# Kernel optimization log

Hardware: AMD Instinct MI355X
Metric: run time of the kernel (lower is better)

## Reference

```python
import jax, jax.numpy as jnp
import numpy as np

B, N, DEG = 64, 256, 16          # graphs, nodes per graph, avg degree
FIN, OUT, DEP, HID = 256, 256, 64, 256
E = B * N * DEG                   # 262144 edges (no self loops)
NN = B * N                        # 16384 total nodes


def setup_inputs() -> dict:
    key = jax.random.key(0)
    ks = jax.random.split(key, 12)
    s = 0.05
    x = jax.random.normal(ks[0], (NN, FIN), jnp.float32)
    # random edges within each graph block, guaranteed no self loops
    src = jax.random.randint(ks[1], (E,), 0, N)
    dst = (src + jax.random.randint(ks[2], (E,), 1, N)) % N
    gid = jnp.repeat(jnp.arange(B) * N, N * DEG)
    edge_index = jnp.stack([src + gid, dst + gid]).astype(jnp.int32)
    edge_attr = jax.random.normal(ks[3], (E, DEP), jnp.float32)
    WA = jax.random.normal(ks[4], (OUT, FIN), jnp.float32) * s
    WB = jax.random.normal(ks[5], (OUT, DEP), jnp.float32) * s
    gcn_bias = jnp.zeros((OUT,), jnp.float32)

    def gru_p(k, insz):
        k1, k2, k3, k4 = jax.random.split(k, 4)
        return (jax.random.normal(k1, (3 * HID, insz), jnp.float32) * s,
                jax.random.normal(k2, (3 * HID, HID), jnp.float32) * s,
                jax.random.normal(k3, (3 * HID,), jnp.float32) * s,
                jax.random.normal(k4, (3 * HID,), jnp.float32) * s)

    w_ih0, w_hh0, b_ih0, b_hh0 = gru_p(ks[6], OUT)
    w_ih1, w_hh1, b_ih1, b_hh1 = gru_p(ks[7], HID)
    w_ih2, w_hh2, b_ih2, b_hh2 = gru_p(ks[8], HID)
    lin_W = jax.random.normal(ks[9], (2, 5 * HID), jnp.float32) * s
    lin_b = jnp.zeros((2,), jnp.float32)
    return dict(x=x, edge_attr=edge_attr, edge_index=edge_index, WA=WA, WB=WB,
                gcn_bias=gcn_bias,
                w_ih0=w_ih0, w_hh0=w_hh0, b_ih0=b_ih0, b_hh0=b_hh0,
                w_ih1=w_ih1, w_hh1=w_hh1, b_ih1=b_ih1, b_hh1=b_hh1,
                w_ih2=w_ih2, w_hh2=w_hh2, b_ih2=b_ih2, b_hh2=b_hh2,
                lin_W=lin_W, lin_b=lin_b)


def _gru_layer(seq, w_ih, w_hh, b_ih, b_hh):
    # seq: [B, T, in] -> ([B, T, HID], final h [B, HID]); torch GRU gate math
    xp = jnp.einsum('bti,gi->btg', seq, w_ih) + b_ih  # precompute input projections

    def step(h, xt):
        gh = h @ w_hh.T + b_hh
        xr, xz, xn = jnp.split(xt, 3, axis=-1)
        hr, hz, hn = jnp.split(gh, 3, axis=-1)
        r = jax.nn.sigmoid(xr + hr)
        z = jax.nn.sigmoid(xz + hz)
        n = jnp.tanh(xn + r * hn)
        h = (1.0 - z) * n + z * h
        return h, h

    h0 = jnp.zeros((seq.shape[0], HID), seq.dtype)
    hT, ys = jax.lax.scan(step, h0, jnp.swapaxes(xp, 0, 1))
    return jnp.swapaxes(ys, 0, 1), hT


def _forward(x, edge_attr, WA, WB, gcn_bias,
             w_ih0, w_hh0, b_ih0, b_hh0,
             w_ih1, w_hh1, b_ih1, b_hh1,
             w_ih2, w_hh2, b_ih2, b_hh2,
             lin_W, lin_b, edge_index):
    # --- myGCNConv: add_remaining_self_loops (none exist), degree norm ---
    loop = jnp.arange(NN, dtype=edge_index.dtype)
    row = jnp.concatenate([edge_index[0], loop])
    col = jnp.concatenate([edge_index[1], loop])
    ea = jnp.concatenate([edge_attr, jnp.ones((NN, DEP), edge_attr.dtype)], axis=0)
    deg = jax.ops.segment_sum(jnp.ones(row.shape, x.dtype), col, num_segments=NN)
    dinv = jnp.where(deg > 0, deg ** -0.5, 0.0)
    norm = dinv[row] * dinv[col]
    # message: norm * tanh(A(x_j) * B(edge_attr)); project nodes once, gather
    Ax = (x @ WA.T)[row]                       # [E+NN, OUT]
    Be = ea @ WB.T                             # [E+NN, OUT]
    msg = norm[:, None] * jnp.tanh(Ax * Be)
    # aggr='mean': scatter-sum / incoming-degree (>=1 after self loops)
    agg = jax.ops.segment_sum(msg, col, num_segments=NN) / jnp.maximum(deg, 1.0)[:, None]
    node = jnp.tanh(agg + gcn_bias)            # model-level Tanh

    # --- GRU (3 layers) over per-graph node sequences (equal lengths) ---
    seq = node.reshape(B, N, OUT)
    hts = []
    for p in ((w_ih0, w_hh0, b_ih0, b_hh0),
              (w_ih1, w_hh1, b_ih1, b_hh1),
              (w_ih2, w_hh2, b_ih2, b_hh2)):
        seq, hT = _gru_layer(seq, *p)
        hts.append(hT)

    avg_pool = seq.sum(axis=1) / N
    max_pool = seq.max(axis=1)
    pool = jnp.concatenate(hts + [max_pool, avg_pool], axis=1)  # [B, 5*HID]
    return jax.nn.softmax(pool @ lin_W.T + lin_b, axis=1)


def reference(x, edge_attr, edge_index, WA, WB, gcn_bias,
              w_ih0, w_hh0, b_ih0, b_hh0,
              w_ih1, w_hh1, b_ih1, b_hh1,
              w_ih2, w_hh2, b_ih2, b_hh2,
              lin_W, lin_b):
    return _forward(x, edge_attr, WA, WB, gcn_bias,
                    w_ih0, w_hh0, b_ih0, b_hh0,
                    w_ih1, w_hh1, b_ih1, b_hh1,
                    w_ih2, w_hh2, b_ih2, b_hh2,
                    lin_W, lin_b, edge_index)
```

## Files before the change

### kernel.cpp

```cpp
#include <hip/hip_runtime.h>
#include <math.h>

#define NN   16384
#define NE   262144
#define NB   64
#define SEQT 256
#define DEP  64
#define DOUT 256
#define G3   768
#define ECAP 64
#define CVTB 21136

typedef _Float16 h2_t   __attribute__((ext_vector_type(2)));
typedef _Float16 f16x4  __attribute__((ext_vector_type(4)));
typedef _Float16 f16x8  __attribute__((ext_vector_type(8)));
typedef float    f32x4  __attribute__((ext_vector_type(4)));

static __device__ __forceinline__ h2_t pk(float a, float b) {
    return (h2_t)__builtin_amdgcn_cvt_pkrtz(a, b);
}

static __device__ __forceinline__ float fast_sigmoid(float v) {
    return __builtin_amdgcn_rcpf(1.f + __expf(-v));
}
static __device__ __forceinline__ float fast_tanh(float v) {
    return 1.f - 2.f * __builtin_amdgcn_rcpf(1.f + __expf(2.f * v));
}

static __device__ __forceinline__ void bar_lds() {
    asm volatile("s_waitcnt lgkmcnt(0)\n\ts_barrier" ::: "memory");
}

__global__ void k_count(const int* __restrict__ ei, int* deg) {
    int e = blockIdx.x * 256 + threadIdx.x;
    if (e < NE) atomicAdd(&deg[ei[NE + e]], 1);
}

__global__ __launch_bounds__(1024) void k_scan_offs(const int* __restrict__ deg,
                                                    int* __restrict__ offs,
                                                    float* __restrict__ dinv) {
    __shared__ int lds[1024];
    const int tid = threadIdx.x;
    const int v0 = tid * 16;
    int loc[16];
    int s = 0;
#pragma unroll
    for (int i = 0; i < 16; ++i) {
        int d = deg[v0 + i];
        loc[i] = s;
        s += d;
        dinv[v0 + i] = rsqrtf((float)(d + 1));
    }
    lds[tid] = s;
    __syncthreads();
    for (int off = 1; off < 1024; off <<= 1) {
        int x = (tid >= off) ? lds[tid - off] : 0;
        __syncthreads();
        lds[tid] += x;
        __syncthreads();
    }
    int base = lds[tid] - s;
#pragma unroll
    for (int i = 0; i < 16; ++i) offs[v0 + i] = base + loc[i];
}

__global__ void k_fill(const int* __restrict__ ei, const int* __restrict__ offs,
                       int* cursor, int* __restrict__ eidx) {
    int e = blockIdx.x * 256 + threadIdx.x;
    if (e < NE) {
        int c = ei[NE + e];
        int pos = offs[c] + atomicAdd(&cursor[c], 1);
        eidx[pos] = e;
    }
}

__global__ void k_cvt_all(const float* __restrict__ x,  const float* __restrict__ wa,
                          const float* __restrict__ w0, const float* __restrict__ w1,
                          const float* __restrict__ w2, const float* __restrict__ ea,
                          const float* __restrict__ wb,
                          _Float16* __restrict__ xo,  _Float16* __restrict__ wao,
                          _Float16* __restrict__ w0o, _Float16* __restrict__ w1o,
                          _Float16* __restrict__ w2o, _Float16* __restrict__ eao,
                          _Float16* __restrict__ wbo,
                          float* __restrict__ Bself,
                          const float* __restrict__ bi0, const float* __restrict__ bh0,
                          const float* __restrict__ bi1, const float* __restrict__ bh1,
                          const float* __restrict__ bi2, const float* __restrict__ bh2,
                          float* __restrict__ bias768) {
    if (blockIdx.x >= CVTB) {
        const int pb = blockIdx.x - CVTB;
        if (pb == 0) {
            int f = threadIdx.x;
            float s = 0.f;
#pragma unroll
            for (int d = 0; d < DEP; ++d) s += wb[f * DEP + d];
            Bself[f] = s;
            return;
        }
        int j = (pb - 1) * 256 + threadIdx.x;
        int l = j / G3, r = j % G3;
        const float* bi = (l == 0) ? bi0 : (l == 1) ? bi1 : bi2;
        const float* bh = (l == 0) ? bh0 : (l == 1) ? bh1 : bh2;
        bias768[j] = bi[r] + (r < 512 ? bh[r] : 0.f);
        return;
    }
    size_t i = ((size_t)blockIdx.x * 256 + threadIdx.x) * 4;
    const size_t B0 = 4194304;
    const size_t B1 = B0 + 65536;
    const size_t B2 = B1 + 196608;
    const size_t B3 = B2 + 196608;
    const size_t B4 = B3 + 196608;
    const size_t B5 = B4 + 16777216;
    const float* in; _Float16* out; size_t off;
    if      (i < B0) { in = x;  out = xo;  off = i; }
    else if (i < B1) { in = wa; out = wao; off = i - B0; }
    else if (i < B2) { in = w0; out = w0o; off = i - B1; }
    else if (i < B3) { in = w1; out = w1o; off = i - B2; }
    else if (i < B4) { in = w2; out = w2o; off = i - B3; }
    else if (i < B5) { in = ea; out = eao; off = i - B4; }
    else             { in = wb; out = wbo; off = i - B5; }
    float4 v = *(const float4*)(in + off);
    *(h2_t*)(out + off)     = pk(v.x, v.y);
    *(h2_t*)(out + off + 2) = pk(v.z, v.w);
}

template <int K, bool F16OUT>
__global__ __launch_bounds__(256) void k_gemm16(const _Float16* __restrict__ A16,
                                                const _Float16* __restrict__ B16,
                                                const float* __restrict__ bias,
                                                void* __restrict__ Cout,
                                                int M, int N) {
    const int tid  = threadIdx.x;
    const int lane = tid & 63;
    const int wv   = tid >> 6;
    const int m0   = blockIdx.x * 128 + wv * 32;
    const int n0   = blockIdx.y * 128;
    const int ml   = lane & 15;
    const int quad = lane >> 4;

    const _Float16* ap0 = A16 + (size_t)(m0 + ml) * K + quad * 8;
    const _Float16* ap1 = ap0 + (size_t)16 * K;
    const _Float16* bp0 = B16 + (size_t)(n0 + ml) * K + quad * 8;

    f32x4 acc[2][8];
#pragma unroll
    for (int i = 0; i < 2; ++i)
#pragma unroll
        for (int j = 0; j < 8; ++j) acc[i][j] = (f32x4){0.f, 0.f, 0.f, 0.f};

#pragma unroll 2
    for (int k0 = 0; k0 < K; k0 += 32) {
        f16x8 a0 = *(const f16x8*)(ap0 + k0);
        f16x8 a1 = *(const f16x8*)(ap1 + k0);
#pragma unroll
        for (int nf = 0; nf < 8; ++nf) {
            f16x8 bf = *(const f16x8*)(bp0 + (size_t)nf * 16 * K + k0);
            acc[0][nf] = __builtin_amdgcn_mfma_f32_16x16x32_f16(a0, bf, acc[0][nf], 0, 0, 0);
            acc[1][nf] = __builtin_amdgcn_mfma_f32_16x16x32_f16(a1, bf, acc[1][nf], 0, 0, 0);
        }
    }

#pragma unroll
    for (int mf = 0; mf < 2; ++mf)
#pragma unroll
        for (int nf = 0; nf < 8; ++nf) {
            const int col = n0 + nf * 16 + ml;
            const float bv = bias ? bias[col] : 0.f;
#pragma unroll
            for (int r = 0; r < 4; ++r) {
                const int row = m0 + mf * 16 + quad * 4 + r;
                float v = acc[mf][nf][r] + bv;
                if (F16OUT)
                    ((_Float16*)Cout)[(size_t)row * N + col] = (_Float16)v;
                else
                    ((float*)Cout)[(size_t)row * N + col] = v;
            }
        }
}

__global__ __launch_bounds__(256) void k_gcn(const float* __restrict__ Ax,
                                             const _Float16* __restrict__ Be16,
                                             const int* __restrict__ ei,
                                             const int* __restrict__ eidx,
                                             const int* __restrict__ offs,
                                             const int* __restrict__ deg,
                                             const float* __restrict__ dinv,
                                             const float* __restrict__ Bself,
                                             const float* __restrict__ gcn_bias,
                                             _Float16* __restrict__ node16) {
    const int v = blockIdx.x;
    const int f = threadIdx.x;

    __shared__ int   es_s[ECAP];
    __shared__ int   src_s[ECAP];
    __shared__ float nrm_s[ECAP];

    const int   base = offs[v];
    const int   cnt  = deg[v];
    const float dv   = dinv[v];
    float acc = 0.f;

    for (int c0 = 0; c0 < cnt; c0 += ECAP) {
        const int n = min(ECAP, cnt - c0);
        if (f < n) {
            int e = eidx[base + c0 + f];
            es_s[f] = e;
            int s = ei[e];
            src_s[f] = s;
            nrm_s[f] = dinv[s] * dv;
        }
        __syncthreads();
#pragma unroll 4
        for (int i = 0; i < n; ++i) {
            float ax = Ax[(size_t)src_s[i] * DOUT + f];
            float be = (float)Be16[(size_t)es_s[i] * DOUT + f];
            acc = fmaf(nrm_s[i], fast_tanh(ax * be), acc);
        }
        __syncthreads();
    }
    acc += dv * dv * fast_tanh(Ax[(size_t)v * DOUT + f] * Bself[f]);
    float nv = fast_tanh(acc / (float)(cnt + 1) + gcn_bias[f]);
    node16[(size_t)v * DOUT + f] = (_Float16)nv;
}

__global__ __launch_bounds__(512, 2) void k_gru_scan(const _Float16* __restrict__ xp16,
                                                     const float* __restrict__ w_hh,
                                                     const float* __restrict__ b_hh,
                                                     _Float16* __restrict__ y16,
                                                     float* __restrict__ hT_all,
                                                     int layer,
                                                     const float* __restrict__ lin_W,
                                                     const float* __restrict__ lin_b,
                                                     float* __restrict__ out) {
    const int tid  = threadIdx.x;
    const int b    = blockIdx.x;
    const int lane = tid & 63;
    const int wv   = tid >> 6;
    const int m    = lane & 15;
    const int quad = lane >> 4;
    const int p    = (m >> 3) & 1;
    const int rsel = m & 3;
    const int j    = wv * 32 + p * 16 + quad * 4 + rsel;
    const bool wr  = (m & 4) == 0;

    f16x8 A[6][8];
#pragma unroll
    for (int rb = 0; rb < 6; ++rb) {
        const int lr  = rb * 16 + m;
        const int row = ((lr >> 5) << 8) + wv * 32 + (lr & 31);
#pragma unroll
        for (int kt = 0; kt < 8; ++kt) {
            const float* wp = w_hh + (size_t)row * 256 + kt * 32 + quad * 8;
            float4 a0 = *(const float4*)wp;
            float4 a1 = *(const float4*)(wp + 4);
            union { f16x8 v; h2_t h[4]; } u;
            u.h[0] = pk(a0.x, a0.y); u.h[1] = pk(a0.z, a0.w);
            u.h[2] = pk(a1.x, a1.y); u.h[3] = pk(a1.z, a1.w);
            A[rb][kt] = u.v;
        }
    }

    const float bhn = b_hh[512 + j];

    __shared__ _Float16 h16[2][256];
    __shared__ float    pool[1280];
    __shared__ float    red[512];

    float h_old = 0.f;
    if (tid < 256) h16[0][tid] = (_Float16)0.f;
    __syncthreads();

    const _Float16* xpb  = xp16 + (size_t)b * SEQT * G3;
    _Float16*       yb16 = y16  + (size_t)b * SEQT * DOUT;

    float mx = -1e30f, sm = 0.f;

    _Float16 pxr = xpb[j], pxz = xpb[256 + j], pxn = xpb[512 + j];

    for (int t = 0; t < SEQT; ++t) {
        const float xr = (float)pxr;
        const float xz = (float)pxz;
        const float xn = (float)pxn;
        {
            const _Float16* xq = xpb + (size_t)(t + 1) * G3 + j;
            pxr = xq[0]; pxz = xq[256]; pxn = xq[512];
        }

        const _Float16* hcur = h16[t & 1];
        f32x4 C[6];
#pragma unroll
        for (int rb = 0; rb < 6; ++rb) C[rb] = (f32x4){0.f, 0.f, 0.f, 0.f};

#pragma unroll
        for (int kt = 0; kt < 8; ++kt) {
            union { f16x8 v; float4 f; } Bk;
            Bk.f = *(const float4*)&hcur[kt * 32 + quad * 8];
#pragma unroll
            for (int rb = 0; rb < 6; ++rb)
                C[rb] = __builtin_amdgcn_mfma_f32_16x16x32_f16(A[rb][kt], Bk.v, C[rb], 0, 0, 0);
        }

        float gh[3];
#pragma unroll
        for (int g = 0; g < 3; ++g) {
            const float lo01 = (rsel & 1) ? C[2 * g][1] : C[2 * g][0];
            const float lo23 = (rsel & 1) ? C[2 * g][3] : C[2 * g][2];
            const float lo   = (rsel & 2) ? lo23 : lo01;
            const float hi01 = (rsel & 1) ? C[2 * g + 1][1] : C[2 * g + 1][0];
            const float hi23 = (rsel & 1) ? C[2 * g + 1][3] : C[2 * g + 1][2];
            const float hi   = (rsel & 2) ? hi23 : hi01;
            gh[g] = p ? hi : lo;
        }

        const float r  = fast_sigmoid(xr + gh[0]);
        const float z  = fast_sigmoid(xz + gh[1]);
        const float n  = fast_tanh(xn + r * (gh[2] + bhn));
        const float hn = n + z * (h_old - n);
        h_old = hn;
        if (wr) {
            h16[(t & 1) ^ 1][j] = (_Float16)hn;
            if (layer < 2) {
                yb16[(size_t)t * DOUT + j] = (_Float16)hn;
                if (t == SEQT - 1) hT_all[layer * NB * 256 + b * 256 + j] = hn;
            }
        }
        if (layer == 2) { mx = fmaxf(mx, hn); sm += hn; }

        bar_lds();
    }

    if (layer == 2) {
        if (wr) {
            pool[j]        = hT_all[b * 256 + j];
            pool[256 + j]  = hT_all[NB * 256 + b * 256 + j];
            pool[512 + j]  = h_old;
            pool[768 + j]  = mx;
            pool[1024 + j] = sm * (1.f / 256.f);
        }
        __syncthreads();
        if (tid < 256) {
            float p0 = 0.f, p1 = 0.f;
            for (int i = tid; i < 1280; i += 256) {
                float pv = pool[i];
                p0 = fmaf(lin_W[i], pv, p0);
                p1 = fmaf(lin_W[1280 + i], pv, p1);
            }
            red[tid] = p0; red[256 + tid] = p1;
        }
        __syncthreads();
        if (tid == 0) {
            float l0 = lin_b[0], l1 = lin_b[1];
            for (int i = 0; i < 256; ++i) { l0 += red[i]; l1 += red[256 + i]; }
            float m2 = fmaxf(l0, l1);
            float e0 = __expf(l0 - m2), e1 = __expf(l1 - m2);
            float s = e0 + e1;
            out[b * 2 + 0] = e0 / s;
            out[b * 2 + 1] = e1 / s;
        }
    }
}

extern "C" void kernel_launch(void* const* d_in, const int* in_sizes, int n_in,
                              void* d_out, int out_size, void* d_ws, size_t ws_size,
                              hipStream_t stream) {
    const float* x         = (const float*)d_in[0];
    const float* edge_attr = (const float*)d_in[1];
    const int*   ei        = (const int*)d_in[2];
    const float* WA        = (const float*)d_in[3];
    const float* WB        = (const float*)d_in[4];
    const float* gcn_bias  = (const float*)d_in[5];
    const float* w_ih[3] = {(const float*)d_in[6],  (const float*)d_in[10], (const float*)d_in[14]};
    const float* w_hh[3] = {(const float*)d_in[7],  (const float*)d_in[11], (const float*)d_in[15]};
    const float* b_ih[3] = {(const float*)d_in[8],  (const float*)d_in[12], (const float*)d_in[16]};
    const float* b_hh[3] = {(const float*)d_in[9],  (const float*)d_in[13], (const float*)d_in[17]};
    const float* lin_W = (const float*)d_in[18];
    const float* lin_b = (const float*)d_in[19];
    float* out = (float*)d_out;

    char* p = (char*)d_ws;
    auto alloc = [&](size_t bytes) {
        char* r = p;
        p += (bytes + 255) & ~(size_t)255;
        return r;
    };
    int*   deg    = (int*)alloc((size_t)NN * 4);
    int*   offs   = (int*)alloc((size_t)NN * 4);
    int*   cursor = (int*)alloc((size_t)NN * 4);
    float* dinv   = (float*)alloc((size_t)NN * 4);
    int*   eidx   = (int*)alloc((size_t)NE * 4);
    float* Bself  = (float*)alloc(256 * 4);
    float* hT     = (float*)alloc(2 * NB * 256 * 4);
    float* bias768 = (float*)alloc(3 * G3 * 4);
    float* Ax     = (float*)alloc((size_t)NN * DOUT * 4);
    _Float16* xp16 = (_Float16*)alloc((size_t)NN * G3 * 2);

    _Float16* node16 = (_Float16*)alloc((size_t)NN * DOUT * 2);
    _Float16* yA16   = (_Float16*)alloc((size_t)NN * DOUT * 2);
    _Float16* x16    = (_Float16*)alloc((size_t)NN * DOUT * 2);
    _Float16* yB16   = x16;
    _Float16* WA16   = (_Float16*)alloc((size_t)256 * 256 * 2);
    _Float16* wih16[3];
    for (int l = 0; l < 3; ++l) wih16[l] = (_Float16*)alloc((size_t)G3 * 256 * 2);
    _Float16* ea16 = (_Float16*)alloc((size_t)NE * DEP * 2);
    _Float16* WB16 = (_Float16*)alloc((size_t)256 * DEP * 2);
    _Float16* Be16 = (_Float16*)alloc((size_t)NE * DOUT * 2);

    hipMemsetAsync(deg, 0, (size_t)3 * NN * 4, stream);
    k_count<<<NE / 256, 256, 0, stream>>>(ei, deg);
    k_scan_offs<<<1, 1024, 0, stream>>>(deg, offs, dinv);
    k_fill<<<NE / 256, 256, 0, stream>>>(ei, offs, cursor, eidx);
    k_cvt_all<<<CVTB + 10, 256, 0, stream>>>(x, WA, w_ih[0], w_ih[1], w_ih[2],
                                             edge_attr, WB,
                                             x16, WA16, wih16[0], wih16[1], wih16[2],
                                             ea16, WB16,
                                             Bself,
                                             b_ih[0], b_hh[0], b_ih[1], b_hh[1],
                                             b_ih[2], b_hh[2], bias768);

    {
        dim3 g(NN / 128, 256 / 128);
        k_gemm16<256, false><<<g, 256, 0, stream>>>(x16, WA16, nullptr, Ax, NN, 256);
    }
    {
        dim3 g(NE / 128, 256 / 128);
        k_gemm16<64, true><<<g, 256, 0, stream>>>(ea16, WB16, nullptr, Be16, NE, 256);
    }
    k_gcn<<<NN, 256, 0, stream>>>(Ax, Be16, ei, eidx, offs, deg, dinv,
                                  Bself, gcn_bias, node16);

    const _Float16* in16 = node16;
    _Float16* y16_outs[3] = {yA16, yB16, yA16};
    for (int l = 0; l < 3; ++l) {
        dim3 g(NN / 128, G3 / 128);
        k_gemm16<256, true><<<g, 256, 0, stream>>>(in16, wih16[l], bias768 + l * G3,
                                                   xp16, NN, G3);
        k_gru_scan<<<NB, 512, 0, stream>>>(xp16, w_hh[l], b_hh[l], y16_outs[l],
                                           hT, l, lin_W, lin_b, out);
        in16 = y16_outs[l];
    }
}
```

Measured before the change: 1.255 ms.

## Replace MFMA recurrent matvec in GRU scan with per-thread fdot2 dot products

The GRU recurrent matrix-vector product moves from MFMA tiles to scalar packed-half dot products. Each pair of threads owns one hidden unit, holds 128 columns of the r/z/n weight rows in registers and combines its partial sums with a lane shuffle. This removes the MFMA tile padding and the lane-select shuffling needed to pull results out of the accumulators. In exchange it issues many more VALU dot instructions per step and needs about 192 packed registers of weights per thread.

```diff
diff --git a/kernel.cpp b/kernel.cpp
--- a/kernel.cpp
+++ b/kernel.cpp
@@ -26,6 +26,18 @@
 static __device__ __forceinline__ float fast_tanh(float v) {
     return 1.f - 2.f * __builtin_amdgcn_rcpf(1.f + __expf(2.f * v));
 }
+
+#if defined(__has_builtin)
+#  if __has_builtin(__builtin_amdgcn_fdot2)
+#    define HAS_FDOT2 1
+#  endif
+#endif
+#ifdef HAS_FDOT2
+#define DOT2(acc, a, b) (acc = __builtin_amdgcn_fdot2((a), (b), (acc), false))
+#else
+#define DOT2(acc, a, b) (acc = fmaf((float)(a)[0], (float)(b)[0], \
+                               fmaf((float)(a)[1], (float)(b)[1], (acc))))
+#endif
 
 static __device__ __forceinline__ void bar_lds() {
     asm volatile("s_waitcnt lgkmcnt(0)\n\ts_barrier" ::: "memory");
@@ -234,37 +246,31 @@
                                                      float* __restrict__ out) {
     const int tid  = threadIdx.x;
     const int b    = blockIdx.x;
-    const int lane = tid & 63;
-    const int wv   = tid >> 6;
-    const int m    = lane & 15;
-    const int quad = lane >> 4;
-    const int p    = (m >> 3) & 1;
-    const int rsel = m & 3;
-    const int j    = wv * 32 + p * 16 + quad * 4 + rsel;
-    const bool wr  = (m & 4) == 0;
-
-    f16x8 A[6][8];
-#pragma unroll
-    for (int rb = 0; rb < 6; ++rb) {
-        const int lr  = rb * 16 + m;
-        const int row = ((lr >> 5) << 8) + wv * 32 + (lr & 31);
-#pragma unroll
-        for (int kt = 0; kt < 8; ++kt) {
-            const float* wp = w_hh + (size_t)row * 256 + kt * 32 + quad * 8;
-            float4 a0 = *(const float4*)wp;
-            float4 a1 = *(const float4*)(wp + 4);
-            union { f16x8 v; h2_t h[4]; } u;
-            u.h[0] = pk(a0.x, a0.y); u.h[1] = pk(a0.z, a0.w);
-            u.h[2] = pk(a1.x, a1.y); u.h[3] = pk(a1.z, a1.w);
-            A[rb][kt] = u.v;
+    const int j    = tid >> 1;
+    const int half = tid & 1;
+    const bool wr  = (half == 0);
+
+    h2_t Wr[64], Wz[64], Wn[64];
+    {
+        const float* pr = w_hh + (size_t)j * 256 + half * 128;
+        const float* pz = pr + (size_t)256 * 256;
+        const float* pn = pz + (size_t)256 * 256;
+#pragma unroll
+        for (int q = 0; q < 32; ++q) {
+            float4 a = *(const float4*)(pr + q * 4);
+            Wr[q * 2] = pk(a.x, a.y); Wr[q * 2 + 1] = pk(a.z, a.w);
+            float4 c = *(const float4*)(pz + q * 4);
+            Wz[q * 2] = pk(c.x, c.y); Wz[q * 2 + 1] = pk(c.z, c.w);
+            float4 d = *(const float4*)(pn + q * 4);
+            Wn[q * 2] = pk(d.x, d.y); Wn[q * 2 + 1] = pk(d.z, d.w);
         }
     }
 
     const float bhn = b_hh[512 + j];
 
-    __shared__ _Float16 h16[2][256];
-    __shared__ float    pool[1280];
-    __shared__ float    red[512];
+    __shared__ __align__(16) _Float16 h16[2][256];
+    __shared__ float pool[1280];
+    __shared__ float red[512];
 
     float h_old = 0.f;
     if (tid < 256) h16[0][tid] = (_Float16)0.f;
@@ -286,35 +292,27 @@
             pxr = xq[0]; pxz = xq[256]; pxn = xq[512];
         }
 
-        const _Float16* hcur = h16[t & 1];
-        f32x4 C[6];
-#pragma unroll
-        for (int rb = 0; rb < 6; ++rb) C[rb] = (f32x4){0.f, 0.f, 0.f, 0.f};
-
-#pragma unroll
-        for (int kt = 0; kt < 8; ++kt) {
-            union { f16x8 v; float4 f; } Bk;
-            Bk.f = *(const float4*)&hcur[kt * 32 + quad * 8];
-#pragma unroll
-            for (int rb = 0; rb < 6; ++rb)
-                C[rb] = __builtin_amdgcn_mfma_f32_16x16x32_f16(A[rb][kt], Bk.v, C[rb], 0, 0, 0);
-        }
-
-        float gh[3];
-#pragma unroll
-        for (int g = 0; g < 3; ++g) {
-            const float lo01 = (rsel & 1) ? C[2 * g][1] : C[2 * g][0];
-            const float lo23 = (rsel & 1) ? C[2 * g][3] : C[2 * g][2];
-            const float lo   = (rsel & 2) ? lo23 : lo01;
-            const float hi01 = (rsel & 1) ? C[2 * g + 1][1] : C[2 * g + 1][0];
-            const float hi23 = (rsel & 1) ? C[2 * g + 1][3] : C[2 * g + 1][2];
-            const float hi   = (rsel & 2) ? hi23 : hi01;
-            gh[g] = p ? hi : lo;
-        }
-
-        const float r  = fast_sigmoid(xr + gh[0]);
-        const float z  = fast_sigmoid(xz + gh[1]);
-        const float n  = fast_tanh(xn + r * (gh[2] + bhn));
+        const f16x8* hv = (const f16x8*)(h16[t & 1]) + half * 16;
+        float ar0 = 0.f, ar1 = 0.f, az0 = 0.f, az1 = 0.f, an0 = 0.f, an1 = 0.f;
+#pragma unroll
+        for (int c = 0; c < 16; ++c) {
+            f16x8 h8 = hv[c];
+            const h2_t* hp = (const h2_t*)&h8;
+            DOT2(ar0, Wr[4 * c + 0], hp[0]); DOT2(ar1, Wr[4 * c + 1], hp[1]);
+            DOT2(az0, Wz[4 * c + 0], hp[0]); DOT2(az1, Wz[4 * c + 1], hp[1]);
+            DOT2(an0, Wn[4 * c + 0], hp[0]); DOT2(an1, Wn[4 * c + 1], hp[1]);
+            DOT2(ar0, Wr[4 * c + 2], hp[2]); DOT2(ar1, Wr[4 * c + 3], hp[3]);
+            DOT2(az0, Wz[4 * c + 2], hp[2]); DOT2(az1, Wz[4 * c + 3], hp[3]);
+            DOT2(an0, Wn[4 * c + 2], hp[2]); DOT2(an1, Wn[4 * c + 3], hp[3]);
+        }
+        const float prt = ar0 + ar1, pzt = az0 + az1, pnt = an0 + an1;
+        const float ghr = prt + __shfl_xor(prt, 1);
+        const float ghz = pzt + __shfl_xor(pzt, 1);
+        const float ghn = pnt + __shfl_xor(pnt, 1);
+
+        const float r  = fast_sigmoid(xr + ghr);
+        const float z  = fast_sigmoid(xz + ghz);
+        const float n  = fast_tanh(xn + r * (ghn + bhn));
         const float hn = n + z * (h_old - n);
         h_old = hn;
         if (wr) {
```

Result: slower. 1.404 ms (+11.8%).
